# Optimization experiments

Measured on AMD Instinct MI355X. Metric: run time of the kernel, lower is better.

The kernel has to match this reference:

```python
import jax, jax.numpy as jnp
import numpy as np

B, T = 512, 64
STOCH, DETER, HIDDEN = 30, 200, 200
A, EMBED = 12, 1024
MIN_STD = 0.1
UPDATE_BIAS = -1.0


def _linear_init(key, fan_in, fan_out):
    w_key, b_key = jax.random.split(key)
    lim = 1.0 / np.sqrt(fan_in)
    W = jax.random.uniform(w_key, (fan_in, fan_out), minval=-lim, maxval=lim, dtype=jnp.float32)
    b = jax.random.uniform(b_key, (fan_out,), minval=-lim, maxval=lim, dtype=jnp.float32)
    return W, b


def setup_inputs() -> dict:
    key = jax.random.key(0)
    ks = jax.random.split(key, 12)
    embed = jax.random.normal(ks[0], (B, T, EMBED), dtype=jnp.float32)
    action = jax.random.normal(ks[1], (B, T, A), dtype=jnp.float32)
    noise_prior = jax.random.normal(ks[2], (B, T, STOCH), dtype=jnp.float32)
    noise_post = jax.random.normal(ks[3], (B, T, STOCH), dtype=jnp.float32)
    inp_W, inp_b = _linear_init(ks[4], STOCH + A, HIDDEN)          # _inp_layers
    gru_W, gru_b = _linear_init(ks[5], HIDDEN + DETER, 3 * DETER)  # GRUCell._layer
    img_out_W, img_out_b = _linear_init(ks[6], DETER, HIDDEN)      # _img_out_layers
    ims_W, ims_b = _linear_init(ks[7], HIDDEN, 2 * STOCH)          # _ims_stat_layer
    obs_out_W, obs_out_b = _linear_init(ks[8], DETER + EMBED, HIDDEN)  # _obs_out_layers
    obs_W, obs_b = _linear_init(ks[9], HIDDEN, 2 * STOCH)          # _obs_stat_layer
    return dict(embed=embed, action=action, noise_prior=noise_prior, noise_post=noise_post,
                inp_W=inp_W, inp_b=inp_b, gru_W=gru_W, gru_b=gru_b,
                img_out_W=img_out_W, img_out_b=img_out_b, ims_W=ims_W, ims_b=ims_b,
                obs_out_W=obs_out_W, obs_out_b=obs_out_b, obs_W=obs_W, obs_b=obs_b)


def _observe(embed, action, noise_prior, noise_post,
             inp_W, inp_b, gru_W, gru_b, img_out_W, img_out_b,
             ims_W, ims_b, obs_out_W, obs_out_b, obs_W, obs_b):
    # time-major for scan: [T, B, ...]
    emb_t = jnp.swapaxes(embed, 0, 1)
    act_t = jnp.swapaxes(action, 0, 1)
    npr_t = jnp.swapaxes(noise_prior, 0, 1)
    npo_t = jnp.swapaxes(noise_post, 0, 1)

    def step(carry, xs):
        stoch, deter = carry                    # posterior stoch [B,STOCH], deter [B,DETER]
        a, e, nz_pr, nz_po = xs
        # img_step: input MLP
        x = jax.nn.elu(jnp.concatenate([stoch, a], -1) @ inp_W + inp_b)
        # GRUCell (norm=False)
        parts = jnp.concatenate([x, deter], -1) @ gru_W + gru_b   # [B, 3*DETER]
        reset, cand, update = jnp.split(parts, 3, -1)
        reset = jax.nn.sigmoid(reset)
        cand = jnp.tanh(reset * cand)
        update = jax.nn.sigmoid(update + UPDATE_BIAS)
        deter_new = update * cand + (1.0 - update) * deter
        # prior stats
        h = jax.nn.elu(deter_new @ img_out_W + img_out_b)
        mean_pr, std_pr = jnp.split(h @ ims_W + ims_b, 2, -1)
        std_pr = jax.nn.softplus(std_pr) + MIN_STD
        stoch_pr = mean_pr + std_pr * nz_pr
        # posterior (temp_post=True): cat(deter, embed)
        ho = jax.nn.elu(jnp.concatenate([deter_new, e], -1) @ obs_out_W + obs_out_b)
        mean_po, std_po = jnp.split(ho @ obs_W + obs_b, 2, -1)
        std_po = jax.nn.softplus(std_po) + MIN_STD
        stoch_po = mean_po + std_po * nz_po
        out = (stoch_po, mean_po, std_po, stoch_pr, mean_pr, std_pr, deter_new)
        return (stoch_po, deter_new), out

    init = (jnp.zeros((B, STOCH), jnp.float32), jnp.zeros((B, DETER), jnp.float32))
    _, outs = jax.lax.scan(step, init, (act_t, emb_t, npr_t, npo_t))
    # back to batch-major and pack into a single array [B, T, 6*STOCH + DETER]
    outs = [jnp.swapaxes(o, 0, 1) for o in outs]
    return jnp.concatenate(outs, -1)


def reference(embed, action, noise_prior, noise_post,
              inp_W, inp_b, gru_W, gru_b, img_out_W, img_out_b,
              ims_W, ims_b, obs_out_W, obs_out_b, obs_W, obs_b):
    return _observe(embed, action, noise_prior, noise_post,
                    inp_W, inp_b, gru_W, gru_b, img_out_W, img_out_b,
                    ims_W, ims_b, obs_out_W, obs_out_b, obs_W, obs_b)
```

## Files before the change

### kernel.cpp

```cpp
#include <hip/hip_runtime.h>

typedef _Float16 h2   __attribute__((ext_vector_type(2)));
typedef _Float16 h4   __attribute__((ext_vector_type(4)));
typedef _Float16 half8 __attribute__((ext_vector_type(8)));
typedef float f32x4   __attribute__((ext_vector_type(4)));

#define MFMA16(a,b,c) __builtin_amdgcn_mfma_f32_16x16x32_f16((a),(b),(c),0,0,0)
#define ATOMIC_ST(p,v) __hip_atomic_store((p),(v),__ATOMIC_RELAXED,__HIP_MEMORY_SCOPE_AGENT)
#define ATOMIC_LD(p)   __hip_atomic_load((p),__ATOMIC_RELAXED,__HIP_MEMORY_SCOPE_AGENT)
#define BAR_LDS() do { asm volatile("s_waitcnt lgkmcnt(0)" ::: "memory"); \
                       __builtin_amdgcn_s_barrier();                      \
                       asm volatile("" ::: "memory"); } while (0)


#define EP_HALVES ((size_t)32768*200)

__global__ void prep_frags(const float* __restrict__ inpW, const float* __restrict__ gruW,
                           const float* __restrict__ imgW, const float* __restrict__ obsoutW,
                           const float* __restrict__ imsW, const float* __restrict__ obsW,
                           _Float16* __restrict__ frags) {
    int gb = blockIdx.x, lane = threadIdx.x;
    const float* src; int KS, K, N, ld, roff = 0, local;
    if (gb < 26)       { src = inpW;    KS = 2;  K = 42;   N = 200; ld = 200; local = gb; }
    else if (gb < 520) { src = gruW;    KS = 13; K = 400;  N = 600; ld = 600; local = gb - 26; }
    else if (gb < 611) { src = imgW;    KS = 7;  K = 200;  N = 200; ld = 200; local = gb - 520; }
    else if (gb < 702) { src = obsoutW; KS = 7;  K = 200;  N = 200; ld = 200; local = gb - 611; }
    else if (gb < 730) { src = imsW;    KS = 7;  K = 200;  N = 60;  ld = 60;  local = gb - 702; }
    else if (gb < 758) { src = obsW;    KS = 7;  K = 200;  N = 60;  ld = 60;  local = gb - 730; }
    else               { src = obsoutW; KS = 32; K = 1024; N = 200; ld = 200; roff = 200; local = gb - 758; }
    int nt = local / KS, ks = local % KS;
    int n  = nt * 16 + (lane & 15);
    int k0 = ks * 32 + (lane >> 4) * 8;
    half8 v;
#pragma unroll
    for (int j = 0; j < 8; ++j) {
        int k = k0 + j;
        float f = (k < K && n < N) ? src[(size_t)(k + roff) * ld + n] : 0.0f;
        v[j] = (_Float16)f;
    }
    *(half8*)(frags + (size_t)gb * 512 + lane * 8) = v;
}

__global__ __launch_bounds__(256) void ep_gemm(const float* __restrict__ embed,
                                               const _Float16* __restrict__ w2f,
                                               _Float16* __restrict__ ep) {
    __shared__ __align__(16) _Float16 aE[16 * 1048];
    int tid = threadIdx.x;
    int rb = blockIdx.x * 16;
#pragma unroll
    for (int i = 0; i < 16; ++i) {
        float4 e = *((const float4*)(embed + (size_t)(rb + i) * 1024) + tid);
        h4 hv; hv[0] = (_Float16)e.x; hv[1] = (_Float16)e.y; hv[2] = (_Float16)e.z; hv[3] = (_Float16)e.w;
        *(h4*)(aE + i * 1048 + tid * 4) = hv;
    }
    __syncthreads();
    int w = tid >> 6, lane = tid & 63, m = lane & 15, q = lane >> 4;
    f32x4 acc[4] = {};
    int nts[4]; int ntc = 0;
    for (int nt = w; nt < 13; nt += 4) nts[ntc++] = nt;
    half8 bb[2][4];
#pragma unroll
    for (int j = 0; j < 4; ++j) if (j < ntc)
        bb[0][j] = *(const half8*)(w2f + ((size_t)(nts[j] * 32) * 64 + lane) * 8);
#pragma unroll
    for (int ks = 0; ks < 32; ++ks) {
        int cur = ks & 1, nxt = cur ^ 1;
        if (ks < 31) {
#pragma unroll
            for (int j = 0; j < 4; ++j) if (j < ntc)
                bb[nxt][j] = *(const half8*)(w2f + ((size_t)(nts[j] * 32 + ks + 1) * 64 + lane) * 8);
        }
        half8 a = *(const half8*)(aE + m * 1048 + ks * 32 + q * 8);
#pragma unroll
        for (int j = 0; j < 4; ++j) if (j < ntc)
            acc[j] = MFMA16(a, bb[cur][j], acc[j]);
    }
    for (int j = 0; j < ntc; ++j) {
        int col = nts[j] * 16 + m;
        if (col < 200) {
#pragma unroll
            for (int i = 0; i < 4; ++i)
                ep[(size_t)(rb + q * 4 + i) * 200 + col] = (_Float16)acc[j][i];
        }
    }
}

__device__ __forceinline__ float sigm_(float x) { return 1.0f / (1.0f + __expf(-x)); }
__device__ __forceinline__ float tanh_(float x) { float e = __expf(2.0f * x); return 1.0f - 2.0f / (e + 1.0f); }
__device__ __forceinline__ float elu_(float x)  { return x > 0.0f ? x : __expf(x) - 1.0f; }
__device__ __forceinline__ float sp_(float x)   { return fmaxf(x, 0.0f) + log1pf(__expf(-fabsf(x))); }
__device__ __forceinline__ unsigned packh2(float a, float b) {
    h2 p; p[0] = (_Float16)a; p[1] = (_Float16)b;
    return __builtin_bit_cast(unsigned, p);
}

__global__ __launch_bounds__(512) __attribute__((amdgpu_waves_per_eu(2, 2))) void rssm_scan(
    const float* __restrict__ action, const float* __restrict__ npr, const float* __restrict__ npo,
    const float* __restrict__ inp_b, const float* __restrict__ gru_b,
    const float* __restrict__ img_b, const float* __restrict__ obsout_b,
    const float* __restrict__ ims_b, const float* __restrict__ obs_b,
    const _Float16* __restrict__ frags, const _Float16* __restrict__ ep,
    unsigned* __restrict__ qdet, unsigned* __restrict__ flags,
    float* __restrict__ out) {

    __shared__ __align__(16) unsigned actI[16 * 36];
    __shared__ __align__(16) unsigned actG[16 * 212];
    __shared__ __align__(16) unsigned actX[16 * 116];
    __shared__ __align__(16) _Float16 parts[16 * 212];
    __shared__ float statspre[16 * 65];
    __shared__ float bias[1320];

    const _Float16* Finp  = frags;
    const _Float16* Fgru  = frags + (size_t)26  * 512;
    const _Float16* Fimg  = frags + (size_t)520 * 512;
    const _Float16* Fobsd = frags + (size_t)611 * 512;
    const _Float16* Fims  = frags + (size_t)702 * 512;
    const _Float16* Fobs  = frags + (size_t)730 * 512;

    const int tid = threadIdx.x, w = tid >> 6, lane = tid & 63, m = lane & 15, q = lane >> 4;
    const int g = blockIdx.x & 31, wg = blockIdx.x >> 5;
    const int rb = g * 16;
    const int colA = w * 16 + m;
    const int colB = (8 + w) * 16 + m;
    unsigned* gf = flags + g * 512;

    for (int i = tid; i < 1320; i += 512) {
        float v;
        if (i < 200) v = inp_b[i];
        else if (i < 800)  v = gru_b[i - 200];
        else if (i < 1000) v = img_b[i - 800];
        else if (i < 1200) v = obsout_b[i - 1000];
        else if (i < 1260) v = ims_b[i - 1200];
        else               v = obs_b[i - 1260];
        bias[i] = v;
    }
    for (int i = tid; i < 16 * 36;  i += 512) actI[i] = 0u;
    for (int i = tid; i < 16 * 212; i += 512) actG[i] = 0u;
    for (int i = tid; i < 16 * 116; i += 512) actX[i] = 0u;

    if (wg < 4) {
        half8 bgru0[13];
        {
            int tA = (w < 4) ? (3 * wg + w) : (12 + 3 * wg + (w - 4));
#pragma unroll
            for (int ks = 0; ks < 13; ++ks)
                bgru0[ks] = *(const half8*)(Fgru + ((size_t)(tA * 13 + ks) * 64 + lane) * 8);
        }
        half8 bgru1[13];
        if (w < 4) {
            int tB = 25 + 3 * wg + w;
#pragma unroll
            for (int ks = 0; ks < 13; ++ks)
                bgru1[ks] = *(const half8*)(Fgru + ((size_t)(tB * 13 + ks) * 64 + lane) * 8);
        }
        half8 bi0[2], bi1[2];
#pragma unroll
        for (int ks = 0; ks < 2; ++ks)
            bi0[ks] = *(const half8*)(Finp + ((size_t)(w * 2 + ks) * 64 + lane) * 8);
        if (w < 5) {
#pragma unroll
            for (int ks = 0; ks < 2; ++ks)
                bi1[ks] = *(const half8*)(Finp + ((size_t)((8 + w) * 2 + ks) * 64 + lane) * 8);
        }
        half8 bp3a[7];
#pragma unroll
        for (int ks = 0; ks < 7; ++ks)
            bp3a[ks] = *(const half8*)(Fobsd + ((size_t)(w * 7 + ks) * 64 + lane) * 8);
        half8 bp4[7];
        if (w >= 4) {
#pragma unroll
            for (int ks = 0; ks < 7; ++ks)
                bp4[ks] = *(const half8*)(Fobs + ((size_t)((w - 4) * 7 + ks) * 64 + lane) * 8);
        }
        __syncthreads();

        unsigned wg4pf = 0u;
        for (int t = 0; t < 64; ++t) {
            h2 epA[4], epB[4];
            if (!(m & 1)) {
#pragma unroll
                for (int i = 0; i < 4; ++i)
                    epA[i] = *(const h2*)(ep + ((size_t)(rb + q * 4 + i) * 64 + t) * 200 + colA);
                if (w < 5 && colB < 200) {
#pragma unroll
                    for (int i = 0; i < 4; ++i)
                        epB[i] = *(const h2*)(ep + ((size_t)(rb + q * 4 + i) * 64 + t) * 200 + colB);
                }
            }
            float2 a2 = make_float2(0.0f, 0.0f);
            if (tid < 96) {
                int r = tid / 6, cp = tid % 6;
                a2 = *(const float2*)(action + ((size_t)(rb + r) * 64 + t) * 12 + 2 * cp);
            }
            float2 nz = make_float2(0.0f, 0.0f);
            if (tid < 240) {
                int r = tid / 15, cp = tid % 15;
                nz = *(const float2*)(npo + ((size_t)(rb + r) * 64 + t) * 30 + 2 * cp);
            }
            if (t >= 2 && tid == 3 && wg4pf < (unsigned)(t - 1)) {
                int it = 0;
                unsigned v = ATOMIC_LD(gf + 508);
                while (v < (unsigned)(t - 1)) {
                    __builtin_amdgcn_s_sleep(1);
                    v = ATOMIC_LD(gf + 508);
                    if (++it > (1 << 20)) break;
                }
                wg4pf = v;
            }
            if (tid < 96) {
                int r = tid / 6, cp = tid % 6;
                actI[r * 36 + 15 + cp] = packh2(a2.x, a2.y);
            }
            BAR_LDS();

            {
                f32x4 acc = {}, acc2 = {};
#pragma unroll
                for (int ks = 0; ks < 2; ++ks) {
                    half8 a = *(const half8*)(actI + m * 36 + ks * 16 + q * 4);
                    acc = MFMA16(a, bi0[ks], acc);
                    if (w < 5) acc2 = MFMA16(a, bi1[ks], acc2);
                }
                f32x4 accN;
#pragma unroll
                for (int i = 0; i < 4; ++i) accN[i] = __shfl_xor(acc[i], 1);
                if (!(m & 1)) {
                    int col = w * 16 + m;
#pragma unroll
                    for (int i = 0; i < 4; ++i)
                        actG[(q * 4 + i) * 212 + (col >> 1)] =
                            packh2(elu_(acc[i] + bias[col]), elu_(accN[i] + bias[col + 1]));
                }
                if (w < 5) {
                    f32x4 acc2N;
#pragma unroll
                    for (int i = 0; i < 4; ++i) acc2N[i] = __shfl_xor(acc2[i], 1);
                    if (!(m & 1)) {
                        int col = (8 + w) * 16 + m;
                        if (col < 200) {
#pragma unroll
                            for (int i = 0; i < 4; ++i)
                                actG[(q * 4 + i) * 212 + (col >> 1)] =
                                    packh2(elu_(acc2[i] + bias[col]), elu_(acc2N[i] + bias[col + 1]));
                        }
                    }
                }
            }
            BAR_LDS();

            {
                f32x4 a0 = {}, a1 = {};
#pragma unroll
                for (int ks = 0; ks < 13; ++ks) {
                    half8 a = *(const half8*)(actG + m * 212 + ks * 16 + q * 4);
                    a0 = MFMA16(a, bgru0[ks], a0);
                    if (w < 4) a1 = MFMA16(a, bgru1[ks], a1);
                }
#pragma unroll
                for (int i = 0; i < 4; ++i)
                    parts[(q * 4 + i) * 212 + w * 16 + m] = (_Float16)a0[i];
                if (w < 4) {
#pragma unroll
                    for (int i = 0; i < 4; ++i)
                        parts[(q * 4 + i) * 212 + (8 + w) * 16 + m] = (_Float16)a1[i];
                }
            }
            half8 pf3[7];
            if (w < 5) {
#pragma unroll
                for (int ks = 0; ks < 7; ++ks)
                    pf3[ks] = *(const half8*)(Fobsd + ((size_t)((8 + w) * 7 + ks) * 64 + lane) * 8);
            }
            BAR_LDS();

            unsigned* qd = qdet + (size_t)((t & 1) * 32 + g) * 1600;
            float gdn0 = 0.0f, gdn1 = 0.0f; int gr = 0, gn0 = 0;
            if (tid < 400) {
                int r = tid / 25, p = tid % 25;
                int n0 = 50 * wg + 2 * p;
                float pg[3][2];
#pragma unroll
                for (int j = 0; j < 3; ++j) {
                    int cg = n0 + 200 * j;
                    int bj = (j == 0) ? 3 * wg : (j == 1) ? 12 + 3 * wg : 25 + 3 * wg;
                    int lt = 4 * j + (cg >> 4) - bj;
                    h2 v = *(const h2*)(parts + r * 212 + lt * 16 + (cg & 15));
                    pg[j][0] = (float)v[0] + bias[200 + cg];
                    pg[j][1] = (float)v[1] + bias[200 + cg + 1];
                }
                h2 dold = *(const h2*)&actG[r * 212 + 100 + (n0 >> 1)];
                float dn[2];
#pragma unroll
                for (int e = 0; e < 2; ++e) {
                    float reset = sigm_(pg[0][e]);
                    float cand  = tanh_(reset * pg[1][e]);
                    float upd   = sigm_(pg[2][e] - 1.0f);
                    dn[e] = upd * cand + (1.0f - upd) * (float)dold[e];
                }
                unsigned pk = packh2(dn[0], dn[1]);
                actG[r * 212 + 100 + (n0 >> 1)] = pk;
                ATOMIC_ST(qd + r * 100 + (n0 >> 1), pk);
                gdn0 = dn[0]; gdn1 = dn[1]; gr = r; gn0 = n0;
            }
            __syncthreads();

            __atomic_signal_fence(__ATOMIC_RELEASE);
            if (tid == 0) ATOMIC_ST(gf + t * 8 + wg, (unsigned)(t + 1));
            if (tid < 400)
                *(float2*)(out + ((size_t)(rb + gr) * 64 + t) * 380 + 180 + gn0) = make_float2(gdn0, gdn1);
            if (tid < 3) {
                unsigned* f = gf + t * 8 + ((wg + 1 + tid) & 3);
                int it = 0;
                while (ATOMIC_LD(f) != (unsigned)(t + 1)) {
                    __builtin_amdgcn_s_sleep(1);
                    if (++it > (1 << 20)) break;
                }
            }
            BAR_LDS();
            __atomic_signal_fence(__ATOMIC_ACQUIRE);
            for (int i = tid; i < 1200; i += 512) {
                int r = i / 75, idx = i % 75;
                int pp = (25 * (wg + 1) + idx) % 100;
                actG[r * 212 + 100 + pp] = ATOMIC_LD(qd + r * 100 + pp);
            }
            if (tid == 3) wg4pf = ATOMIC_LD(gf + 508);
            BAR_LDS();

            {
                f32x4 acc = {}, acc2 = {};
#pragma unroll
                for (int ks = 0; ks < 7; ++ks) {
                    half8 a = *(const half8*)(actG + m * 212 + 100 + ks * 16 + q * 4);
                    acc = MFMA16(a, bp3a[ks], acc);
                    if (w < 5) acc2 = MFMA16(a, pf3[ks], acc2);
                }
                f32x4 accN;
#pragma unroll
                for (int i = 0; i < 4; ++i) accN[i] = __shfl_xor(acc[i], 1);
                if (!(m & 1)) {
#pragma unroll
                    for (int i = 0; i < 4; ++i)
                        actX[(q * 4 + i) * 116 + (colA >> 1)] =
                            packh2(elu_(acc[i] + bias[1000 + colA] + (float)epA[i][0]),
                                   elu_(accN[i] + bias[1000 + colA + 1] + (float)epA[i][1]));
                }
                if (w < 5) {
                    f32x4 acc2N;
#pragma unroll
                    for (int i = 0; i < 4; ++i) acc2N[i] = __shfl_xor(acc2[i], 1);
                    if (!(m & 1) && colB < 200) {
#pragma unroll
                        for (int i = 0; i < 4; ++i)
                            actX[(q * 4 + i) * 116 + (colB >> 1)] =
                                packh2(elu_(acc2[i] + bias[1000 + colB] + (float)epB[i][0]),
                                       elu_(acc2N[i] + bias[1000 + colB + 1] + (float)epB[i][1]));
                    }
                }
            }
            BAR_LDS();

            if (w >= 4) {
                f32x4 acc = {};
#pragma unroll
                for (int ks = 0; ks < 7; ++ks) {
                    half8 a = *(const half8*)(actX + m * 116 + ks * 16 + q * 4);
                    acc = MFMA16(a, bp4[ks], acc);
                }
#pragma unroll
                for (int i = 0; i < 4; ++i)
                    statspre[(q * 4 + i) * 65 + (w - 4) * 16 + m] = acc[i];
            }
            BAR_LDS();

            if (tid < 240) {
                int r = tid / 15, cp = tid % 15;
                float m0 = statspre[r * 65 + 2 * cp]     + bias[1260 + 2 * cp];
                float m1 = statspre[r * 65 + 2 * cp + 1] + bias[1260 + 2 * cp + 1];
                float s0 = sp_(statspre[r * 65 + 30 + 2 * cp]     + bias[1260 + 30 + 2 * cp]) + 0.1f;
                float s1 = sp_(statspre[r * 65 + 30 + 2 * cp + 1] + bias[1260 + 30 + 2 * cp + 1]) + 0.1f;
                float st0 = m0 + s0 * nz.x, st1 = m1 + s1 * nz.y;
                actI[r * 36 + cp] = packh2(st0, st1);
                if (wg == 2) {
                    size_t ob = ((size_t)(rb + r) * 64 + t) * 380;
                    *(float2*)(out + ob + 2 * cp)      = make_float2(st0, st1);
                    *(float2*)(out + ob + 30 + 2 * cp) = make_float2(m0, m1);
                    *(float2*)(out + ob + 60 + 2 * cp) = make_float2(s0, s1);
                }
            }
        }
    } else {
        half8 bp3a[7];
#pragma unroll
        for (int ks = 0; ks < 7; ++ks)
            bp3a[ks] = *(const half8*)(Fimg + ((size_t)(w * 7 + ks) * 64 + lane) * 8);
        half8 bp3b[7];
        if (w < 5) {
#pragma unroll
            for (int ks = 0; ks < 7; ++ks)
                bp3b[ks] = *(const half8*)(Fimg + ((size_t)((8 + w) * 7 + ks) * 64 + lane) * 8);
        }
        half8 bp4[7];
        if (w >= 4) {
#pragma unroll
            for (int ks = 0; ks < 7; ++ks)
                bp4[ks] = *(const half8*)(Fims + ((size_t)((w - 4) * 7 + ks) * 64 + lane) * 8);
        }
        __syncthreads();

        for (int t = 0; t < 64; ++t) {
            float2 nz = make_float2(0.0f, 0.0f);
            if (tid < 240) {
                int r = tid / 15, cp = tid % 15;
                nz = *(const float2*)(npr + ((size_t)(rb + r) * 64 + t) * 30 + 2 * cp);
            }
            if (tid < 4) {
                unsigned* f = gf + t * 8 + tid;
                int it = 0;
                while (ATOMIC_LD(f) != (unsigned)(t + 1)) {
                    __builtin_amdgcn_s_sleep(1);
                    if (++it > (1 << 20)) break;
                }
            }
            BAR_LDS();
            __atomic_signal_fence(__ATOMIC_ACQUIRE);
            const unsigned* qd = qdet + (size_t)((t & 1) * 32 + g) * 1600;
            for (int i = tid; i < 1600; i += 512)
                actG[(i / 100) * 212 + 100 + (i % 100)] = ATOMIC_LD(qd + i);
            BAR_LDS();
            __atomic_signal_fence(__ATOMIC_RELEASE);
            if (tid == 0) ATOMIC_ST(gf + 508, (unsigned)(t + 1));

            {
                f32x4 acc = {}, acc2 = {};
#pragma unroll
                for (int ks = 0; ks < 7; ++ks) {
                    half8 a = *(const half8*)(actG + m * 212 + 100 + ks * 16 + q * 4);
                    acc = MFMA16(a, bp3a[ks], acc);
                    if (w < 5) acc2 = MFMA16(a, bp3b[ks], acc2);
                }
                f32x4 accN;
#pragma unroll
                for (int i = 0; i < 4; ++i) accN[i] = __shfl_xor(acc[i], 1);
                if (!(m & 1)) {
#pragma unroll
                    for (int i = 0; i < 4; ++i)
                        actX[(q * 4 + i) * 116 + (colA >> 1)] =
                            packh2(elu_(acc[i] + bias[800 + colA]),
                                   elu_(accN[i] + bias[800 + colA + 1]));
                }
                if (w < 5) {
                    f32x4 acc2N;
#pragma unroll
                    for (int i = 0; i < 4; ++i) acc2N[i] = __shfl_xor(acc2[i], 1);
                    if (!(m & 1) && colB < 200) {
#pragma unroll
                        for (int i = 0; i < 4; ++i)
                            actX[(q * 4 + i) * 116 + (colB >> 1)] =
                                packh2(elu_(acc2[i] + bias[800 + colB]),
                                       elu_(acc2N[i] + bias[800 + colB + 1]));
                    }
                }
            }
            BAR_LDS();

            if (w >= 4) {
                f32x4 acc = {};
#pragma unroll
                for (int ks = 0; ks < 7; ++ks) {
                    half8 a = *(const half8*)(actX + m * 116 + ks * 16 + q * 4);
                    acc = MFMA16(a, bp4[ks], acc);
                }
#pragma unroll
                for (int i = 0; i < 4; ++i)
                    statspre[(q * 4 + i) * 65 + (w - 4) * 16 + m] = acc[i];
            }
            BAR_LDS();

            if (tid < 240) {
                int r = tid / 15, cp = tid % 15;
                float m0 = statspre[r * 65 + 2 * cp]     + bias[1200 + 2 * cp];
                float m1 = statspre[r * 65 + 2 * cp + 1] + bias[1200 + 2 * cp + 1];
                float s0 = sp_(statspre[r * 65 + 30 + 2 * cp]     + bias[1200 + 30 + 2 * cp]) + 0.1f;
                float s1 = sp_(statspre[r * 65 + 30 + 2 * cp + 1] + bias[1200 + 30 + 2 * cp + 1]) + 0.1f;
                float st0 = m0 + s0 * nz.x, st1 = m1 + s1 * nz.y;
                size_t ob = ((size_t)(rb + r) * 64 + t) * 380;
                *(float2*)(out + ob + 90 + 2 * cp)  = make_float2(st0, st1);
                *(float2*)(out + ob + 120 + 2 * cp) = make_float2(m0, m1);
                *(float2*)(out + ob + 150 + 2 * cp) = make_float2(s0, s1);
            }
        }
    }
}

extern "C" void kernel_launch(void* const* d_in, const int* in_sizes, int n_in,
                              void* d_out, int out_size, void* d_ws, size_t ws_size,
                              hipStream_t stream) {
    const float* embed   = (const float*)d_in[0];
    const float* action  = (const float*)d_in[1];
    const float* npr     = (const float*)d_in[2];
    const float* npo     = (const float*)d_in[3];
    const float* inpW    = (const float*)d_in[4];
    const float* inpb    = (const float*)d_in[5];
    const float* gruW    = (const float*)d_in[6];
    const float* grub    = (const float*)d_in[7];
    const float* imgW    = (const float*)d_in[8];
    const float* imgb    = (const float*)d_in[9];
    const float* imsW    = (const float*)d_in[10];
    const float* imsb    = (const float*)d_in[11];
    const float* obsoutW = (const float*)d_in[12];
    const float* obsoutb = (const float*)d_in[13];
    const float* obsW    = (const float*)d_in[14];
    const float* obsb    = (const float*)d_in[15];

    char* ws = (char*)d_ws;
    _Float16* ep     = (_Float16*)ws;
    _Float16* frags  = (_Float16*)(ws + EP_HALVES * 2);
    char* p          = ws + EP_HALVES * 2 + (size_t)1174 * 1024;
    unsigned* qdetb  = (unsigned*)p;
    p += (size_t)2 * 32 * 1600 * 4;
    unsigned* flagsb = (unsigned*)p;

    prep_frags<<<1174, 64, 0, stream>>>(inpW, gruW, imgW, obsoutW, imsW, obsW, frags);
    ep_gemm<<<2048, 256, 0, stream>>>(embed, frags + (size_t)758 * 512, ep);
    rssm_scan<<<160, 512, 0, stream>>>(action, npr, npo, inpb, grub, imgb, obsoutb,
                                       imsb, obsb, frags, ep, qdetb, flagsb,
                                       (float*)d_out);
}
```

Measured before the change: 847.7 us.

## Replace flag-based inter-block sync with step-tagged 64-bit data words

Each exchanged deter word is now stored as a 64-bit value carrying the timestep tag in its upper half. Consumers poll the data words directly until every tag matches, which removes the separate flag store and the extra barriers and flag spins in both the GRU producer groups and the consumer group. The exchange buffer doubles in size and is zeroed inside ep_gemm each call. Polling many words adds memory traffic while waiting, and the wait loop still gives up after a fixed iteration count.

```diff
diff --git a/kernel.cpp b/kernel.cpp
--- a/kernel.cpp
+++ b/kernel.cpp
@@ -4,16 +4,20 @@
 typedef _Float16 h4   __attribute__((ext_vector_type(4)));
 typedef _Float16 half8 __attribute__((ext_vector_type(8)));
 typedef float f32x4   __attribute__((ext_vector_type(4)));
+typedef unsigned long long u64;
 
 #define MFMA16(a,b,c) __builtin_amdgcn_mfma_f32_16x16x32_f16((a),(b),(c),0,0,0)
 #define ATOMIC_ST(p,v) __hip_atomic_store((p),(v),__ATOMIC_RELAXED,__HIP_MEMORY_SCOPE_AGENT)
 #define ATOMIC_LD(p)   __hip_atomic_load((p),__ATOMIC_RELAXED,__HIP_MEMORY_SCOPE_AGENT)
+#define ATOMIC_ST64(p,v) __hip_atomic_store((p),(v),__ATOMIC_RELAXED,__HIP_MEMORY_SCOPE_AGENT)
+#define ATOMIC_LD64(p)   __hip_atomic_load((p),__ATOMIC_RELAXED,__HIP_MEMORY_SCOPE_AGENT)
 #define BAR_LDS() do { asm volatile("s_waitcnt lgkmcnt(0)" ::: "memory"); \
                        __builtin_amdgcn_s_barrier();                      \
                        asm volatile("" ::: "memory"); } while (0)
 
 
 #define EP_HALVES ((size_t)32768*200)
+#define ZWORDS64 (102400 + 8192)
 
 __global__ void prep_frags(const float* __restrict__ inpW, const float* __restrict__ gruW,
                            const float* __restrict__ imgW, const float* __restrict__ obsoutW,
@@ -43,7 +47,12 @@
 
 __global__ __launch_bounds__(256) void ep_gemm(const float* __restrict__ embed,
                                                const _Float16* __restrict__ w2f,
-                                               _Float16* __restrict__ ep) {
+                                               _Float16* __restrict__ ep,
+                                               u64* __restrict__ zmem) {
+    {
+        int gid = blockIdx.x * 256 + threadIdx.x;
+        if (gid < ZWORDS64) zmem[gid] = 0ull;
+    }
     __shared__ __align__(16) _Float16 aE[16 * 1048];
     int tid = threadIdx.x;
     int rb = blockIdx.x * 16;
@@ -100,7 +109,7 @@
     const float* __restrict__ img_b, const float* __restrict__ obsout_b,
     const float* __restrict__ ims_b, const float* __restrict__ obs_b,
     const _Float16* __restrict__ frags, const _Float16* __restrict__ ep,
-    unsigned* __restrict__ qdet, unsigned* __restrict__ flags,
+    u64* __restrict__ qdet, unsigned* __restrict__ flags,
     float* __restrict__ out) {
 
     __shared__ __align__(16) unsigned actI[16 * 36];
@@ -273,8 +282,8 @@
             }
             BAR_LDS();
 
-            unsigned* qd = qdet + (size_t)((t & 1) * 32 + g) * 1600;
-            float gdn0 = 0.0f, gdn1 = 0.0f; int gr = 0, gn0 = 0;
+            u64* qd = qdet + (size_t)((t & 1) * 32 + g) * 1600;
+            u64 tagw = (u64)(unsigned)(t + 1) << 32;
             if (tid < 400) {
                 int r = tid / 25, p = tid % 25;
                 int n0 = 50 * wg + 2 * p;
@@ -299,29 +308,33 @@
                 }
                 unsigned pk = packh2(dn[0], dn[1]);
                 actG[r * 212 + 100 + (n0 >> 1)] = pk;
-                ATOMIC_ST(qd + r * 100 + (n0 >> 1), pk);
-                gdn0 = dn[0]; gdn1 = dn[1]; gr = r; gn0 = n0;
-            }
-            __syncthreads();
-
-            __atomic_signal_fence(__ATOMIC_RELEASE);
-            if (tid == 0) ATOMIC_ST(gf + t * 8 + wg, (unsigned)(t + 1));
-            if (tid < 400)
-                *(float2*)(out + ((size_t)(rb + gr) * 64 + t) * 380 + 180 + gn0) = make_float2(gdn0, gdn1);
-            if (tid < 3) {
-                unsigned* f = gf + t * 8 + ((wg + 1 + tid) & 3);
-                int it = 0;
-                while (ATOMIC_LD(f) != (unsigned)(t + 1)) {
-                    __builtin_amdgcn_s_sleep(1);
-                    if (++it > (1 << 20)) break;
-                }
-            }
-            BAR_LDS();
-            __atomic_signal_fence(__ATOMIC_ACQUIRE);
-            for (int i = tid; i < 1200; i += 512) {
-                int r = i / 75, idx = i % 75;
-                int pp = (25 * (wg + 1) + idx) % 100;
-                actG[r * 212 + 100 + pp] = ATOMIC_LD(qd + r * 100 + pp);
+                ATOMIC_ST64(qd + r * 100 + (n0 >> 1), tagw | pk);
+                *(float2*)(out + ((size_t)(rb + r) * 64 + t) * 380 + 180 + n0) = make_float2(dn[0], dn[1]);
+            }
+
+            {
+                unsigned want = (unsigned)(t + 1);
+                int i0 = tid, i1 = tid + 512, i2 = tid + 1024;
+                int r0 = i0 / 75, p0 = (25 * (wg + 1) + i0 % 75) % 100;
+                int r1 = i1 / 75, p1 = (25 * (wg + 1) + i1 % 75) % 100;
+                bool h2ok = i2 < 1200;
+                int r2 = h2ok ? i2 / 75 : 0, p2 = h2ok ? (25 * (wg + 1) + i2 % 75) % 100 : 0;
+                const u64* q0 = qd + r0 * 100 + p0;
+                const u64* q1 = qd + r1 * 100 + p1;
+                const u64* q2 = qd + r2 * 100 + p2;
+                u64 v0, v1, v2; int it = 0;
+                for (;;) {
+                    v0 = ATOMIC_LD64(q0);
+                    v1 = ATOMIC_LD64(q1);
+                    v2 = h2ok ? ATOMIC_LD64(q2) : ((u64)want << 32);
+                    bool ok = ((unsigned)(v0 >> 32) == want) &
+                              ((unsigned)(v1 >> 32) == want) &
+                              ((unsigned)(v2 >> 32) == want);
+                    if (__all(ok) || ++it > (1 << 17)) break;
+                }
+                actG[r0 * 212 + 100 + p0] = (unsigned)v0;
+                actG[r1 * 212 + 100 + p1] = (unsigned)v1;
+                if (h2ok) actG[r2 * 212 + 100 + p2] = (unsigned)v2;
             }
             if (tid == 3) wg4pf = ATOMIC_LD(gf + 508);
             BAR_LDS();
@@ -413,19 +426,28 @@
                 int r = tid / 15, cp = tid % 15;
                 nz = *(const float2*)(npr + ((size_t)(rb + r) * 64 + t) * 30 + 2 * cp);
             }
-            if (tid < 4) {
-                unsigned* f = gf + t * 8 + tid;
-                int it = 0;
-                while (ATOMIC_LD(f) != (unsigned)(t + 1)) {
-                    __builtin_amdgcn_s_sleep(1);
-                    if (++it > (1 << 20)) break;
-                }
-            }
-            BAR_LDS();
-            __atomic_signal_fence(__ATOMIC_ACQUIRE);
-            const unsigned* qd = qdet + (size_t)((t & 1) * 32 + g) * 1600;
-            for (int i = tid; i < 1600; i += 512)
-                actG[(i / 100) * 212 + 100 + (i % 100)] = ATOMIC_LD(qd + i);
+            {
+                unsigned want = (unsigned)(t + 1);
+                const u64* qd = qdet + (size_t)((t & 1) * 32 + g) * 1600;
+                int i0 = tid, i1 = tid + 512, i2 = tid + 1024, i3 = tid + 1536;
+                bool h3 = i3 < 1600;
+                u64 v0, v1, v2, v3; int it = 0;
+                for (;;) {
+                    v0 = ATOMIC_LD64(qd + i0);
+                    v1 = ATOMIC_LD64(qd + i1);
+                    v2 = ATOMIC_LD64(qd + i2);
+                    v3 = h3 ? ATOMIC_LD64(qd + i3) : ((u64)want << 32);
+                    bool ok = ((unsigned)(v0 >> 32) == want) &
+                              ((unsigned)(v1 >> 32) == want) &
+                              ((unsigned)(v2 >> 32) == want) &
+                              ((unsigned)(v3 >> 32) == want);
+                    if (__all(ok) || ++it > (1 << 17)) break;
+                }
+                actG[(i0 / 100) * 212 + 100 + (i0 % 100)] = (unsigned)v0;
+                actG[(i1 / 100) * 212 + 100 + (i1 % 100)] = (unsigned)v1;
+                actG[(i2 / 100) * 212 + 100 + (i2 % 100)] = (unsigned)v2;
+                if (h3) actG[(i3 / 100) * 212 + 100 + (i3 % 100)] = (unsigned)v3;
+            }
             BAR_LDS();
             __atomic_signal_fence(__ATOMIC_RELEASE);
             if (tid == 0) ATOMIC_ST(gf + 508, (unsigned)(t + 1));
@@ -516,12 +538,12 @@
     _Float16* ep     = (_Float16*)ws;
     _Float16* frags  = (_Float16*)(ws + EP_HALVES * 2);
     char* p          = ws + EP_HALVES * 2 + (size_t)1174 * 1024;
-    unsigned* qdetb  = (unsigned*)p;
-    p += (size_t)2 * 32 * 1600 * 4;
+    u64* qdetb       = (u64*)p;
+    p += (size_t)2 * 32 * 1600 * 8;
     unsigned* flagsb = (unsigned*)p;
 
     prep_frags<<<1174, 64, 0, stream>>>(inpW, gruW, imgW, obsoutW, imsW, obsW, frags);
-    ep_gemm<<<2048, 256, 0, stream>>>(embed, frags + (size_t)758 * 512, ep);
+    ep_gemm<<<2048, 256, 0, stream>>>(embed, frags + (size_t)758 * 512, ep, qdetb);
     rssm_scan<<<160, 512, 0, stream>>>(action, npr, npo, inpb, grub, imgb, obsoutb,
                                        imsb, obsb, frags, ep, qdetb, flagsb,
                                        (float*)d_out);
```

Result: slower. 922.9 us (+8.9%).
